# Kernel tuning notes

Measured on AMD Instinct MI355X. Metric: run time of the kernel, lower is better.

## Reference

```python
import jax, jax.numpy as jnp
import numpy as np

B, S, D, F, E = 8, 1024, 1024, 4096, 8
EPS = 1e-5  # fairseq LayerNorm default


def setup_inputs() -> dict:
    key = jax.random.key(0)
    ks = jax.random.split(key, 4)
    s = 0.02
    return {
        "input_features": jax.random.normal(ks[0], (B, S, D), jnp.float32),
        "centroids": jax.random.normal(ks[1], (E, D), jnp.float32) * 0.1,  # orthogonal_ gain=0.1 stand-in
        "ln_g": jnp.ones((E, D), jnp.float32),
        "ln_b": jnp.zeros((E, D), jnp.float32),
        "w1": jax.random.normal(ks[2], (E, D, F), jnp.float32) * s,
        "b1": jnp.zeros((E, F), jnp.float32),
        "w2": jax.random.normal(ks[3], (E, F, D), jnp.float32) * s,  # torch inits ff2 to zero; random here so bwd is non-trivial
        "b2": jnp.zeros((E, D), jnp.float32),
    }


def reference(input_features, centroids, ln_g, ln_b, w1, b1, w2, b2):
    # Single-worker inference path of BaseLayer: greedy top-1 routing, no shuffle,
    # All2All is the identity. sort_by_expert + per-expert blocks + inverse_sort
    # is equivalent to per-token routing, expressed here with a one-hot combine.
    x = input_features.reshape(-1, D)                         # [T, D] tokens
    aff = jax.lax.stop_gradient(x @ centroids.T)              # [T, E] affinities (torch.no_grad)
    eid = jnp.argmax(aff, axis=-1)                            # [T] greedy_assignment k=1

    # alpha = sigmoid(<token, its expert centroid>) -- grads DO flow to centroids here
    alpha = jax.nn.sigmoid(jnp.sum(x * centroids[eid], axis=-1, keepdims=True))  # [T, 1]

    # Per-expert LayerNorm: normalize once, gather per-token gamma/beta
    mu = jnp.mean(x, axis=-1, keepdims=True)
    var = jnp.mean((x - mu) ** 2, axis=-1, keepdims=True)
    xn = (x - mu) * jax.lax.rsqrt(var + EPS)
    xln = xn * ln_g[eid] + ln_b[eid]                          # [T, D]

    # BaseSublayer: xs + ff2(relu(ff1(LN(xs))))
    # combined with alpha gate: out = alpha*sub(x) + (1-alpha)*x = x + alpha*ffn_residual
    onehot = jax.nn.one_hot(eid, E, dtype=x.dtype)            # [T, E] dispatch mask
    ffn = jnp.zeros_like(x)
    for e in range(E):  # small fixed expert loop (structurally distinct weights)
        h = jax.nn.relu(xln @ w1[e] + b1[e])                  # [T, F]
        ffn = ffn + onehot[:, e:e + 1] * (h @ w2[e] + b2[e])  # [T, D]

    out = x + alpha * ffn
    return out.reshape(input_features.shape)
```

## Files before the change

kernel.cpp:

```cpp
#include <hip/hip_runtime.h>

#define NT 8192
#define DIM 1024
#define FDIM 4096
#define NEXP 8

typedef __attribute__((ext_vector_type(8))) short bfx8;
typedef __attribute__((ext_vector_type(4))) float fx4;

__device__ __forceinline__ unsigned short f2bf(float f) {
  union { float f; unsigned u; } v; v.f = f;
  unsigned u = v.u;
  unsigned r = u + 0x7FFFu + ((u >> 16) & 1u);
  return (unsigned short)(r >> 16);
}

__device__ __forceinline__ void gload16(const void* g, void* l) {
  __builtin_amdgcn_global_load_lds(
      (const __attribute__((address_space(1))) unsigned int*)g,
      (__attribute__((address_space(3))) unsigned int*)l, 16, 0, 0);
}

__global__ void k_zero(int* __restrict__ counts) {
  if (threadIdx.x < NEXP) counts[threadIdx.x] = 0;
}

__global__ __launch_bounds__(256) void k_route(
    const float* __restrict__ x, const float* __restrict__ cent,
    const float* __restrict__ g, const float* __restrict__ b,
    int* __restrict__ eid, float* __restrict__ alpha, int* __restrict__ counts,
    unsigned short* __restrict__ xln)
{
  const int wv = threadIdx.x >> 6, lane = threadIdx.x & 63;
  const int t = blockIdx.x * 4 + wv;

  const float4* xr = (const float4*)(x + (size_t)t * DIM);
  float4 xv[4];
#pragma unroll
  for (int j = 0; j < 4; ++j) xv[j] = xr[lane + j * 64];

  float dot[NEXP];
#pragma unroll
  for (int e = 0; e < NEXP; ++e) {
    const float4* cr = (const float4*)(cent + (size_t)e * DIM);
    float d = 0.f;
#pragma unroll
    for (int j = 0; j < 4; ++j) {
      const float4 cv = cr[lane + j * 64];
      d += xv[j].x * cv.x + xv[j].y * cv.y + xv[j].z * cv.z + xv[j].w * cv.w;
    }
    dot[e] = d;
  }
  float s = 0.f, ss = 0.f;
#pragma unroll
  for (int j = 0; j < 4; ++j) {
    s  += xv[j].x + xv[j].y + xv[j].z + xv[j].w;
    ss += xv[j].x * xv[j].x + xv[j].y * xv[j].y + xv[j].z * xv[j].z + xv[j].w * xv[j].w;
  }
#pragma unroll
  for (int off = 1; off < 64; off <<= 1) {
#pragma unroll
    for (int e = 0; e < NEXP; ++e) dot[e] += __shfl_xor(dot[e], off);
    s += __shfl_xor(s, off); ss += __shfl_xor(ss, off);
  }
  int best = 0; float bv = dot[0];
#pragma unroll
  for (int e = 1; e < NEXP; ++e)
    if (dot[e] > bv) { bv = dot[e]; best = e; }
  if (lane == 0) {
    eid[t] = best;
    alpha[t] = 1.0f / (1.0f + expf(-bv));
    atomicAdd(&counts[best], 1);
  }
  const float mu = s * (1.0f / DIM);
  const float var = ss * (1.0f / DIM) - mu * mu;
  const float rstd = rsqrtf(var + 1e-5f);

  const float4* gr = (const float4*)(g + (size_t)best * DIM);
  const float4* br = (const float4*)(b + (size_t)best * DIM);
  ushort4* orow = (ushort4*)(xln + (size_t)t * DIM);
#pragma unroll
  for (int j = 0; j < 4; ++j) {
    const float4 gv = gr[lane + j * 64];
    const float4 bv4 = br[lane + j * 64];
    ushort4 o;
    o.x = f2bf((xv[j].x - mu) * rstd * gv.x + bv4.x);
    o.y = f2bf((xv[j].y - mu) * rstd * gv.y + bv4.y);
    o.z = f2bf((xv[j].z - mu) * rstd * gv.z + bv4.z);
    o.w = f2bf((xv[j].w - mu) * rstd * gv.w + bv4.w);
    orow[lane + j * 64] = o;
  }
}

__global__ void k_scan(const int* __restrict__ counts, int* __restrict__ bs, int* __restrict__ cur) {
  if (threadIdx.x == 0) {
    int s = 0;
    for (int e = 0; e < NEXP; ++e) { bs[e] = s; cur[e] = s; s += counts[e]; }
  }
}

__global__ void k_rowtok(const int* __restrict__ eid, int* __restrict__ cur,
                         int* __restrict__ row_tok) {
  const int t = blockIdx.x * 256 + threadIdx.x;
  const int e = eid[t];
  const int pos = atomicAdd(&cur[e], 1);
  row_tok[pos] = t;
}

__global__ __launch_bounds__(256) void k_transpose(
    const float* __restrict__ in, unsigned short* __restrict__ outT, int R, int C)
{
  __shared__ float T[64 * 128];
  const int e = blockIdx.z;
  const float* src = in + (size_t)e * R * C;
  unsigned short* dst = outT + (size_t)e * R * C;
  const int r0 = blockIdx.y * 64, c0 = blockIdx.x * 128;
  const int t = threadIdx.x, lane = t & 63, wv = t >> 6;
  const int rsub = wv * 2 + (lane >> 5);
  const int cb = (lane & 31) ^ rsub;
#pragma unroll
  for (int i = 0; i < 8; ++i) {
    const int rbase = i * 8 + wv * 2;
    gload16(src + (size_t)(r0 + rbase + (lane >> 5)) * C + c0 + cb * 4,
            &T[rbase * 128]);
  }
  __syncthreads();
  const int q = t >> 5, cbase = t & 31;
#pragma unroll
  for (int it = 0; it < 4; ++it) {
    const int c = cbase + it * 32;
    unsigned short o[8];
#pragma unroll
    for (int u = 0; u < 8; ++u)
      o[u] = f2bf(T[(q * 8 + u) * 128 + ((((c >> 2) ^ u) << 2) | (c & 3))]);
    *(uint4*)(dst + (size_t)(c0 + c) * R + r0 + q * 8) = *(const uint4*)o;
  }
}

template<int K, int N, bool FIRST>
__global__ __launch_bounds__(256) void k_gemm(
    const unsigned short* __restrict__ A,
    const unsigned short* __restrict__ Bt,
    const float* __restrict__ bias,
    const int* __restrict__ bs, const int* __restrict__ counts,
    unsigned short* __restrict__ Hout,
    const int* __restrict__ row_tok, const float* __restrict__ alpha,
    const float* __restrict__ xin, float* __restrict__ out)
{
  const int MB = NT / 128;
  const int bid = blockIdx.x;
  const int e = bid & 7;
  const int l = bid >> 3;
  const int m0 = (l % MB) * 128;
  const int cnt = counts[e];
  if (m0 >= cnt) return;
  const int n0 = (l / MB) * 128;
  const int rbase = bs[e];

  __shared__ __align__(16) char smem[32 * 132 * 4];
  unsigned short* lA = (unsigned short*)smem;
  unsigned short* lB = (unsigned short*)(smem + 8192);
  float* Lf = (float*)smem;

  const int tid = threadIdx.x;
  const int lane = tid & 63, wv = tid >> 6;
  const int wm = (wv >> 1) * 64, wn = (wv & 1) * 64;
  const int lr = lane & 15, lg = lane >> 4;

  fx4 acc[4][4] = {};

  const unsigned short* Bte = Bt + (size_t)e * N * K;

  const unsigned short* aP[2];
  const unsigned short* bP[2];
#pragma unroll
  for (int p = 0; p < 2; ++p) {
    const int g = p * 256 + tid;
    const int row = g >> 2, kq = (g & 3) * 8;
    int ar = rbase + m0 + row;
    ar = ar < NT ? ar : NT - 1;
    if constexpr (FIRST) {
      const int tok = row_tok[ar];
      aP[p] = A + (size_t)tok * K + kq;
    } else {
      aP[p] = A + (size_t)ar * K + kq;
    }
    bP[p] = Bte + (size_t)(n0 + row) * K + kq;
  }

  for (int k0 = 0; k0 < K; k0 += 32) {
    gload16(aP[0] + k0, &lA[(0 * 4 + wv) * 512]);
    gload16(aP[1] + k0, &lA[(1 * 4 + wv) * 512]);
    gload16(bP[0] + k0, &lB[(0 * 4 + wv) * 512]);
    gload16(bP[1] + k0, &lB[(1 * 4 + wv) * 512]);
    __syncthreads();
    bfx8 bf[4];
#pragma unroll
    for (int j = 0; j < 4; ++j)
      bf[j] = *(const bfx8*)(&lB[(wn + j * 16 + lr) * 32 + lg * 8]);
#pragma unroll
    for (int i = 0; i < 4; ++i) {
      const bfx8 af = *(const bfx8*)(&lA[(wm + i * 16 + lr) * 32 + lg * 8]);
#pragma unroll
      for (int j = 0; j < 4; ++j)
        acc[i][j] = __builtin_amdgcn_mfma_f32_16x16x32_bf16(af, bf[j], acc[i][j], 0, 0, 0);
    }
    __syncthreads();
  }

  const float* be = bias + (size_t)e * N;
  float bcol[4];
#pragma unroll
  for (int j = 0; j < 4; ++j) bcol[j] = be[n0 + wn + j * 16 + lr];

#pragma unroll
  for (int i = 0; i < 4; ++i) {
    __syncthreads();
#pragma unroll
    for (int r2 = 0; r2 < 4; ++r2) {
      const int rowp = (wv >> 1) * 16 + lg * 4 + r2;
#pragma unroll
      for (int j = 0; j < 4; ++j) {
        float v = acc[i][j][r2] + bcol[j];
        if (FIRST) v = v > 0.f ? v : 0.f;
        Lf[rowp * 132 + wn + j * 16 + lr] = v;
      }
    }
    __syncthreads();
    if constexpr (FIRST) {
#pragma unroll
      for (int s = 0; s < 2; ++s) {
        const int tsk = tid + 256 * s;
        const int rr = tsk >> 4, cg = tsk & 15;
        const int ra = i * 16 + ((rr >> 4) << 6) + (rr & 15);
        if (m0 + ra < cnt) {
          const float4 a = *(const float4*)&Lf[rr * 132 + cg * 8];
          const float4 b = *(const float4*)&Lf[rr * 132 + cg * 8 + 4];
          unsigned short o[8] = { f2bf(a.x), f2bf(a.y), f2bf(a.z), f2bf(a.w),
                                  f2bf(b.x), f2bf(b.y), f2bf(b.z), f2bf(b.w) };
          *(uint4*)(Hout + (size_t)(rbase + m0 + ra) * N + n0 + cg * 8) =
              *(const uint4*)o;
        }
      }
    } else {
#pragma unroll
      for (int s = 0; s < 4; ++s) {
        const int tsk = tid + 256 * s;
        const int rr = tsk >> 5, c4 = tsk & 31;
        const int ra = i * 16 + ((rr >> 4) << 6) + (rr & 15);
        if (m0 + ra < cnt) {
          const int tok = row_tok[rbase + m0 + ra];
          const float al = alpha[tok];
          const float4 v = *(const float4*)&Lf[rr * 132 + c4 * 4];
          const float4 xr = *(const float4*)(xin + (size_t)tok * N + n0 + c4 * 4);
          float4 o;
          o.x = xr.x + al * v.x;
          o.y = xr.y + al * v.y;
          o.z = xr.z + al * v.z;
          o.w = xr.w + al * v.w;
          *(float4*)(out + (size_t)tok * N + n0 + c4 * 4) = o;
        }
      }
    }
  }
}

extern "C" void kernel_launch(void* const* d_in, const int* in_sizes, int n_in,
                              void* d_out, int out_size, void* d_ws, size_t ws_size,
                              hipStream_t stream)
{
  const float* x    = (const float*)d_in[0];
  const float* cent = (const float*)d_in[1];
  const float* ln_g = (const float*)d_in[2];
  const float* ln_b = (const float*)d_in[3];
  const float* w1   = (const float*)d_in[4];
  const float* b1   = (const float*)d_in[5];
  const float* w2   = (const float*)d_in[6];
  const float* b2   = (const float*)d_in[7];
  float* out = (float*)d_out;

  char* ws = (char*)d_ws;
  unsigned short* xln  = (unsigned short*)(ws);
  unsigned short* hbuf = (unsigned short*)(ws + (16ull << 20));
  unsigned short* w1t  = (unsigned short*)(ws + (80ull << 20));
  unsigned short* w2t  = (unsigned short*)(ws + (144ull << 20));
  char* tail = ws + (208ull << 20);
  int*    eid    = (int*)(tail);
  float*  alpha  = (float*)(tail + 32768);
  int*    rowtok = (int*)(tail + 65536);
  int*    counts = (int*)(tail + 98304);
  int*    basep  = counts + 16;
  int*    cur    = counts + 32;

  k_zero<<<1, 64, 0, stream>>>(counts);
  k_route<<<NT / 4, 256, 0, stream>>>(x, cent, ln_g, ln_b, eid, alpha, counts, xln);
  k_scan<<<1, 1, 0, stream>>>(counts, basep, cur);
  k_rowtok<<<NT / 256, 256, 0, stream>>>(eid, cur, rowtok);
  k_transpose<<<dim3(FDIM / 128, DIM / 64, NEXP), 256, 0, stream>>>(w1, w1t, DIM, FDIM);
  k_transpose<<<dim3(DIM / 128, FDIM / 64, NEXP), 256, 0, stream>>>(w2, w2t, FDIM, DIM);
  k_gemm<DIM, FDIM, true><<<NEXP * (NT / 128) * (FDIM / 128), 256, 0, stream>>>(
      xln, w1t, b1, basep, counts, hbuf, rowtok, nullptr, nullptr, nullptr);
  k_gemm<FDIM, DIM, false><<<NEXP * (NT / 128) * (DIM / 128), 256, 0, stream>>>(
      hbuf, w2t, b2, basep, counts, nullptr, rowtok, alpha, x, out);
}
```

Baseline: 482.0 us.

## Fuse weight transpose and bf16 conversion into the expert GEMM B-tile load

Drops the two standalone transpose kernels that turned the fp32 w1/w2 into transposed bf16 copies before the GEMMs. Each GEMM block now loads fp32 weight tiles straight into LDS in their native layout with an XOR swizzle, then builds the bf16 B fragments by reading eight scalars from LDS and rounding them in registers. This removes a full pass that reads and writes all expert weights plus two launches. In exchange, every M-block re-reads fp32 weights, which is twice the bytes per tile and is repeated across blocks. It also adds LDS reads and conversion ALU work to the inner k-loop.

```diff
diff --git a/kernel.cpp b/kernel.cpp
--- a/kernel.cpp
+++ b/kernel.cpp
@@ -107,40 +107,10 @@
   row_tok[pos] = t;
 }
 
-__global__ __launch_bounds__(256) void k_transpose(
-    const float* __restrict__ in, unsigned short* __restrict__ outT, int R, int C)
-{
-  __shared__ float T[64 * 128];
-  const int e = blockIdx.z;
-  const float* src = in + (size_t)e * R * C;
-  unsigned short* dst = outT + (size_t)e * R * C;
-  const int r0 = blockIdx.y * 64, c0 = blockIdx.x * 128;
-  const int t = threadIdx.x, lane = t & 63, wv = t >> 6;
-  const int rsub = wv * 2 + (lane >> 5);
-  const int cb = (lane & 31) ^ rsub;
-#pragma unroll
-  for (int i = 0; i < 8; ++i) {
-    const int rbase = i * 8 + wv * 2;
-    gload16(src + (size_t)(r0 + rbase + (lane >> 5)) * C + c0 + cb * 4,
-            &T[rbase * 128]);
-  }
-  __syncthreads();
-  const int q = t >> 5, cbase = t & 31;
-#pragma unroll
-  for (int it = 0; it < 4; ++it) {
-    const int c = cbase + it * 32;
-    unsigned short o[8];
-#pragma unroll
-    for (int u = 0; u < 8; ++u)
-      o[u] = f2bf(T[(q * 8 + u) * 128 + ((((c >> 2) ^ u) << 2) | (c & 3))]);
-    *(uint4*)(dst + (size_t)(c0 + c) * R + r0 + q * 8) = *(const uint4*)o;
-  }
-}
-
 template<int K, int N, bool FIRST>
 __global__ __launch_bounds__(256) void k_gemm(
     const unsigned short* __restrict__ A,
-    const unsigned short* __restrict__ Bt,
+    const float* __restrict__ W,
     const float* __restrict__ bias,
     const int* __restrict__ bs, const int* __restrict__ counts,
     unsigned short* __restrict__ Hout,
@@ -157,9 +127,9 @@
   const int n0 = (l / MB) * 128;
   const int rbase = bs[e];
 
-  __shared__ __align__(16) char smem[32 * 132 * 4];
+  __shared__ __align__(16) char smem[24576];
   unsigned short* lA = (unsigned short*)smem;
-  unsigned short* lB = (unsigned short*)(smem + 8192);
+  float* Tf = (float*)(smem + 8192);
   float* Lf = (float*)smem;
 
   const int tid = threadIdx.x;
@@ -169,10 +139,9 @@
 
   fx4 acc[4][4] = {};
 
-  const unsigned short* Bte = Bt + (size_t)e * N * K;
+  const float* We = W + (size_t)e * (size_t)K * N;
 
   const unsigned short* aP[2];
-  const unsigned short* bP[2];
 #pragma unroll
   for (int p = 0; p < 2; ++p) {
     const int g = p * 256 + tid;
@@ -185,19 +154,31 @@
     } else {
       aP[p] = A + (size_t)ar * K + kq;
     }
-    bP[p] = Bte + (size_t)(n0 + row) * K + kq;
-  }
+  }
+
+  const int rsub = wv * 2 + (lane >> 5);
+  const int cb = (lane & 31) ^ rsub;
+  const float* wP = We + (size_t)(wv * 2 + (lane >> 5)) * N + n0 + cb * 4;
 
   for (int k0 = 0; k0 < K; k0 += 32) {
     gload16(aP[0] + k0, &lA[(0 * 4 + wv) * 512]);
     gload16(aP[1] + k0, &lA[(1 * 4 + wv) * 512]);
-    gload16(bP[0] + k0, &lB[(0 * 4 + wv) * 512]);
-    gload16(bP[1] + k0, &lB[(1 * 4 + wv) * 512]);
-    __syncthreads();
+#pragma unroll
+    for (int i = 0; i < 4; ++i)
+      gload16(wP + (size_t)(k0 + i * 8) * N, &Tf[(i * 8 + wv * 2) * 128]);
+    __syncthreads();
+
     bfx8 bf[4];
 #pragma unroll
-    for (int j = 0; j < 4; ++j)
-      bf[j] = *(const bfx8*)(&lB[(wn + j * 16 + lr) * 32 + lg * 8]);
+    for (int j = 0; j < 4; ++j) {
+      const int n = wn + j * 16 + lr;
+      const int nlo = n & 3, nhi = n >> 2;
+      unsigned short tmp[8];
+#pragma unroll
+      for (int u = 0; u < 8; ++u)
+        tmp[u] = f2bf(Tf[(lg * 8 + u) * 128 + (((nhi ^ u) << 2) | nlo)]);
+      bf[j] = *(const bfx8*)tmp;
+    }
 #pragma unroll
     for (int i = 0; i < 4; ++i) {
       const bfx8 af = *(const bfx8*)(&lA[(wm + i * 16 + lr) * 32 + lg * 8]);
@@ -282,8 +263,6 @@
   char* ws = (char*)d_ws;
   unsigned short* xln  = (unsigned short*)(ws);
   unsigned short* hbuf = (unsigned short*)(ws + (16ull << 20));
-  unsigned short* w1t  = (unsigned short*)(ws + (80ull << 20));
-  unsigned short* w2t  = (unsigned short*)(ws + (144ull << 20));
   char* tail = ws + (208ull << 20);
   int*    eid    = (int*)(tail);
   float*  alpha  = (float*)(tail + 32768);
@@ -296,10 +275,8 @@
   k_route<<<NT / 4, 256, 0, stream>>>(x, cent, ln_g, ln_b, eid, alpha, counts, xln);
   k_scan<<<1, 1, 0, stream>>>(counts, basep, cur);
   k_rowtok<<<NT / 256, 256, 0, stream>>>(eid, cur, rowtok);
-  k_transpose<<<dim3(FDIM / 128, DIM / 64, NEXP), 256, 0, stream>>>(w1, w1t, DIM, FDIM);
-  k_transpose<<<dim3(DIM / 128, FDIM / 64, NEXP), 256, 0, stream>>>(w2, w2t, FDIM, DIM);
   k_gemm<DIM, FDIM, true><<<NEXP * (NT / 128) * (FDIM / 128), 256, 0, stream>>>(
-      xln, w1t, b1, basep, counts, hbuf, rowtok, nullptr, nullptr, nullptr);
+      xln, w1, b1, basep, counts, hbuf, rowtok, nullptr, nullptr, nullptr);
   k_gemm<FDIM, DIM, false><<<NEXP * (NT / 128) * (DIM / 128), 256, 0, stream>>>(
-      hbuf, w2t, b2, basep, counts, nullptr, rowtok, alpha, x, out);
-}
+      hbuf, w2, b2, basep, counts, nullptr, rowtok, alpha, x, out);
+}
```

After: 532.0 us. 10.4% more time.
